# Performance work log

Hardware: AMD Instinct MI355X
Metric: run time of the kernel (lower is better)

The kernel has to match this reference:

```python
import jax, jax.numpy as jnp
import numpy as np

BETA = 0.25


def setup_inputs() -> dict:
    key = jax.random.key(0)
    k1, k2 = jax.random.split(key)
    z = jax.random.normal(k1, (32, 256, 32, 32), dtype=jnp.float32)
    codebook = jax.random.normal(k2, (1024, 256), dtype=jnp.float32)
    return {"z": z, "codebook": codebook}


def reference(z, codebook):
    # z: (B, C, H, W) with C == e_dim; codebook: (n_e, e_dim)
    b, c, h, w = z.shape
    z_perm = jnp.transpose(z, (0, 2, 3, 1))          # (B, H, W, C)
    z_flat = z_perm.reshape(-1, c)                   # (N, e_dim)

    d = (jnp.sum(z_flat ** 2, axis=1, keepdims=True)
         + jnp.sum(codebook ** 2, axis=1)
         - 2.0 * z_flat @ codebook.T)                # (N, n_e)

    min_idx = jnp.argmin(d, axis=1)                  # (N,)
    # gather == one-hot @ codebook in the original
    z_q = codebook[min_idx].reshape(z_perm.shape)    # (B, H, W, C)

    sg = jax.lax.stop_gradient
    e_latent_loss = jnp.mean((sg(z_q) - z_perm) ** 2)
    q_latent_loss = jnp.mean((z_q - sg(z_perm)) ** 2)
    codebook_loss = q_latent_loss + e_latent_loss * BETA

    # straight-through estimator
    z_q_st = z_perm + sg(z_q - z_perm)
    z_q_out = jnp.transpose(z_q_st, (0, 3, 1, 2))    # (B, C, H, W)

    indices = min_idx.reshape(b, 1, h, w)
    return z_q_out, codebook_loss, indices
```

## Files before the change

### kernel.cpp

```cpp
#include <hip/hip_runtime.h>


#define EDIM   256
#define NCODE  1024
#define HWSZ   1024
#define NPIX   32768
#define LOSS_OFF 8388608
#define IDX_OFF  8388609
#define THR    0.05f

typedef __attribute__((ext_vector_type(8))) short s16x8;
typedef __attribute__((ext_vector_type(4))) float f32x4;

__device__ inline unsigned short f2bf(float f) {
    unsigned u = __float_as_uint(f);
    return (unsigned short)((u + 0x7FFFu + ((u >> 16) & 1u)) >> 16);
}
__device__ inline float bf2f(unsigned short h) { return __uint_as_float(((unsigned)h) << 16); }

__global__ __launch_bounds__(256) void vq_cbsplit(const float* __restrict__ cb,
                                                  unsigned short* __restrict__ cbs,
                                                  float* __restrict__ cnorm)
{
    const int t    = threadIdx.x;
    const int code = (blockIdx.x << 3) + (t >> 5);
    const int kg   = t & 31;
    const float4 v0 = *(const float4*)(cb + (size_t)code * EDIM + (kg << 3));
    const float4 v1 = *(const float4*)(cb + (size_t)code * EDIM + (kg << 3) + 4);

    float s = v0.x*v0.x + v0.y*v0.y + v0.z*v0.z + v0.w*v0.w
            + v1.x*v1.x + v1.y*v1.y + v1.z*v1.z + v1.w*v1.w;
    s += __shfl_xor(s, 1, 64);  s += __shfl_xor(s, 2, 64);
    s += __shfl_xor(s, 4, 64);  s += __shfl_xor(s, 8, 64);
    s += __shfl_xor(s, 16, 64);
    if (kg == 0) cnorm[code] = s;

    const float f[8] = {v0.x, v0.y, v0.z, v0.w, v1.x, v1.y, v1.z, v1.w};
    unsigned short h[8], l[8];
#pragma unroll
    for (int j = 0; j < 8; ++j) { h[j] = f2bf(f[j]); l[j] = f2bf(f[j] - bf2f(h[j])); }
    uint4 H, L;
    H.x = (unsigned)h[0] | ((unsigned)h[1] << 16);  H.y = (unsigned)h[2] | ((unsigned)h[3] << 16);
    H.z = (unsigned)h[4] | ((unsigned)h[5] << 16);  H.w = (unsigned)h[6] | ((unsigned)h[7] << 16);
    L.x = (unsigned)l[0] | ((unsigned)l[1] << 16);  L.y = (unsigned)l[2] | ((unsigned)l[3] << 16);
    L.z = (unsigned)l[4] | ((unsigned)l[5] << 16);  L.w = (unsigned)l[6] | ((unsigned)l[7] << 16);
    const size_t off = ((size_t)(kg >> 2) * NCODE + code) * 64 + ((size_t)(kg & 3) << 3);
    *(uint4*)(cbs + off)      = H;
    *(uint4*)(cbs + off + 32) = L;
}

__global__ __launch_bounds__(256) void vq_prep(const float* __restrict__ z,
                                               unsigned short* __restrict__ zscH,
                                               unsigned short* __restrict__ zscL,
                                               float* __restrict__ loss_slot)
{
    __shared__ unsigned lzp[64][68];

    const int t  = threadIdx.x;
    const int n0 = blockIdx.x << 6;
    const int bb = n0 >> 10, hw0 = n0 & 1023;
    if (blockIdx.x == 0 && t == 0) *loss_slot = 0.0f;
    const float* zb = z + (size_t)bb * (EDIM * HWSZ) + hw0;

    for (int pk = 0; pk < 4; ++pk) {
#pragma unroll
        for (int i = 0; i < 4; ++i) {
            const int linear = (i << 8) + t;
            const int kk  = linear >> 4;
            const int px4 = (linear & 15) << 2;
            const float4 v = *reinterpret_cast<const float4*>(zb + (pk * 64 + kk) * HWSZ + px4);
            const float vv[4] = {v.x, v.y, v.z, v.w};
#pragma unroll
            for (int j = 0; j < 4; ++j) {
                const unsigned short h = f2bf(vv[j]);
                const unsigned short l = f2bf(vv[j] - bf2f(h));
                lzp[px4 + j][kk] = (unsigned)h | ((unsigned)l << 16);
            }
        }
        __syncthreads();
        {
            const int px = t >> 2, q = t & 3;
            const int kq16 = q << 4;
            const uint4 q0 = *(const uint4*)&lzp[px][kq16];
            const uint4 q1 = *(const uint4*)&lzp[px][kq16 + 4];
            const uint4 q2 = *(const uint4*)&lzp[px][kq16 + 8];
            const uint4 q3 = *(const uint4*)&lzp[px][kq16 + 12];
            #define PH(a,b) (((a) & 0xffffu) | ((b) << 16))
            #define PL(a,b) (((a) >> 16) | ((b) & 0xffff0000u))
            const uint4 hA = {PH(q0.x,q0.y), PH(q0.z,q0.w), PH(q1.x,q1.y), PH(q1.z,q1.w)};
            const uint4 hB = {PH(q2.x,q2.y), PH(q2.z,q2.w), PH(q3.x,q3.y), PH(q3.z,q3.w)};
            const uint4 lA = {PL(q0.x,q0.y), PL(q0.z,q0.w), PL(q1.x,q1.y), PL(q1.z,q1.w)};
            const uint4 lB = {PL(q2.x,q2.y), PL(q2.z,q2.w), PL(q3.x,q3.y), PL(q3.z,q3.w)};
            #undef PH
            #undef PL
            const int kc  = (pk << 1) + (q >> 1);
            const size_t off = ((size_t)kc * NPIX + n0 + px) * 32 + ((q & 1) << 4);
            *(uint4*)(zscH + off)     = hA;
            *(uint4*)(zscH + off + 8) = hB;
            *(uint4*)(zscL + off)     = lA;
            *(uint4*)(zscL + off + 8) = lB;
        }
        __syncthreads();
    }
}

__global__ __launch_bounds__(256, 2) void vq_argmin_g(
    const float* __restrict__ z, const float* __restrict__ cb,
    const unsigned short* __restrict__ zscH, const unsigned short* __restrict__ zscL,
    const unsigned short* __restrict__ cbs, const float* __restrict__ cnorm,
    float* __restrict__ idx_out)
{
    __shared__ unsigned short zh[8][64][32];
    __shared__ unsigned short zl[8][64][32];
    __shared__ float cn[NCODE];
    __shared__ float rb1[4][64], rb2[4][64];
    __shared__ int   ri1[4][64], ri2[4][64];
    __shared__ int   fl_cnt, fl_px[64], fl_i1[64], fl_i2[64];
    __shared__ float fred[2][4];

    const int t    = threadIdx.x;
    const int lane = t & 63;
    const int w    = t >> 6;
    const int n0   = blockIdx.x << 6;
    const int bb   = n0 >> 10, hw0 = n0 & 1023;
    const int l15  = lane & 15, kq = lane >> 4;

#pragma unroll
    for (int i = 0; i < 8; ++i) {
        const int idx = (i << 8) + t;
        const int kc  = idx >> 8;
        const int px  = (idx & 255) >> 2;
        const int q   = idx & 3;
        const size_t so = ((size_t)kc * NPIX + n0 + px) * 32 + (q << 3);
        *(uint4*)&zh[kc][px][q << 3] = *(const uint4*)(zscH + so);
        *(uint4*)&zl[kc][px][q << 3] = *(const uint4*)(zscL + so);
    }
#pragma unroll
    for (int i = 0; i < 4; ++i) cn[(i << 8) + t] = cnorm[(i << 8) + t];
    if (t == 0) fl_cnt = 0;
    __syncthreads();

    float b1[4], b2[4]; int i1[4], i2[4];
#pragma unroll
    for (int nf = 0; nf < 4; ++nf) { b1[nf] = 3.402823e38f; b2[nf] = 3.402823e38f; i1[nf] = 0; i2[nf] = 0; }

    f32x4 acc[4][4];
    const size_t lanebase = ((size_t)((w << 6) + l15) << 6) + (kq << 3);

    s16x8 pA0, pA1, pA2, pA3, pA4, pA5, pA6, pA7;
    s16x8 pB0, pB1, pB2, pB3, pB4, pB5, pB6, pB7;

#define LOADA(d0,d1,d2,d3,d4,d5,d6,d7,S) do {                                   \
        const int g_ = (S) >> 3, kc_ = (S) & 7;                                 \
        const unsigned short* bp = cbs +                                        \
            (((size_t)kc_ * NCODE + (g_ << 8)) << 6) + lanebase;                \
        d0 = *(const s16x8*)(bp);          d1 = *(const s16x8*)(bp + 1024);     \
        d2 = *(const s16x8*)(bp + 2048);   d3 = *(const s16x8*)(bp + 3072);     \
        d4 = *(const s16x8*)(bp + 32);     d5 = *(const s16x8*)(bp + 1056);     \
        d6 = *(const s16x8*)(bp + 2080);   d7 = *(const s16x8*)(bp + 3104);     \
    } while (0)

#define COMPUTE(a0,a1,a2,a3,a4,a5,a6,a7,S) do {                                 \
        const int g_ = (S) >> 3, kc_ = (S) & 7;                                 \
        if (kc_ == 0) {                                                         \
            _Pragma("unroll") for (int mf = 0; mf < 4; ++mf)                    \
            _Pragma("unroll") for (int nf = 0; nf < 4; ++nf)                    \
                acc[mf][nf] = (f32x4){0.f, 0.f, 0.f, 0.f};                      \
        }                                                                       \
        s16x8 bh[4], bl[4];                                                     \
        _Pragma("unroll") for (int nf = 0; nf < 4; ++nf) {                      \
            bh[nf] = *(const s16x8*)&zh[kc_][(nf << 4) + l15][kq << 3];         \
            bl[nf] = *(const s16x8*)&zl[kc_][(nf << 4) + l15][kq << 3];         \
        }                                                                       \
        _Pragma("unroll") for (int nf = 0; nf < 4; ++nf) {                      \
            acc[0][nf] = __builtin_amdgcn_mfma_f32_16x16x32_bf16(a0, bh[nf], acc[0][nf], 0, 0, 0); \
            acc[1][nf] = __builtin_amdgcn_mfma_f32_16x16x32_bf16(a1, bh[nf], acc[1][nf], 0, 0, 0); \
            acc[2][nf] = __builtin_amdgcn_mfma_f32_16x16x32_bf16(a2, bh[nf], acc[2][nf], 0, 0, 0); \
            acc[3][nf] = __builtin_amdgcn_mfma_f32_16x16x32_bf16(a3, bh[nf], acc[3][nf], 0, 0, 0); \
        }                                                                       \
        _Pragma("unroll") for (int nf = 0; nf < 4; ++nf) {                      \
            acc[0][nf] = __builtin_amdgcn_mfma_f32_16x16x32_bf16(a0, bl[nf], acc[0][nf], 0, 0, 0); \
            acc[1][nf] = __builtin_amdgcn_mfma_f32_16x16x32_bf16(a1, bl[nf], acc[1][nf], 0, 0, 0); \
            acc[2][nf] = __builtin_amdgcn_mfma_f32_16x16x32_bf16(a2, bl[nf], acc[2][nf], 0, 0, 0); \
            acc[3][nf] = __builtin_amdgcn_mfma_f32_16x16x32_bf16(a3, bl[nf], acc[3][nf], 0, 0, 0); \
        }                                                                       \
        _Pragma("unroll") for (int nf = 0; nf < 4; ++nf) {                      \
            acc[0][nf] = __builtin_amdgcn_mfma_f32_16x16x32_bf16(a4, bh[nf], acc[0][nf], 0, 0, 0); \
            acc[1][nf] = __builtin_amdgcn_mfma_f32_16x16x32_bf16(a5, bh[nf], acc[1][nf], 0, 0, 0); \
            acc[2][nf] = __builtin_amdgcn_mfma_f32_16x16x32_bf16(a6, bh[nf], acc[2][nf], 0, 0, 0); \
            acc[3][nf] = __builtin_amdgcn_mfma_f32_16x16x32_bf16(a7, bh[nf], acc[3][nf], 0, 0, 0); \
        }                                                                       \
        if (kc_ == 7) {                                                         \
            _Pragma("unroll") for (int mf = 0; mf < 4; ++mf)                    \
            _Pragma("unroll") for (int r = 0; r < 4; ++r) {                     \
                const int local = (w << 6) + (mf << 4) + (kq << 2) + r;         \
                const int code  = (g_ << 8) + local;                            \
                const float cnv = cn[code];                                     \
                _Pragma("unroll") for (int nf = 0; nf < 4; ++nf) {              \
                    const float d = fmaf(-2.f, acc[mf][nf][r], cnv);            \
                    if (d < b1[nf])      { b2[nf] = b1[nf]; i2[nf] = i1[nf]; b1[nf] = d; i1[nf] = code; } \
                    else if (d < b2[nf]) { b2[nf] = d; i2[nf] = code; }         \
                }                                                               \
            }                                                                   \
        }                                                                       \
    } while (0)

    LOADA(pA0,pA1,pA2,pA3,pA4,pA5,pA6,pA7, 0);
    for (int s = 0; s < 32; s += 2) {
        LOADA(pB0,pB1,pB2,pB3,pB4,pB5,pB6,pB7, s + 1);
        COMPUTE(pA0,pA1,pA2,pA3,pA4,pA5,pA6,pA7, s);
        if (s + 2 < 32) LOADA(pA0,pA1,pA2,pA3,pA4,pA5,pA6,pA7, s + 2);
        COMPUTE(pB0,pB1,pB2,pB3,pB4,pB5,pB6,pB7, s + 1);
    }
#undef LOADA
#undef COMPUTE

#pragma unroll
    for (int nf = 0; nf < 4; ++nf) {
        float B1 = b1[nf], B2 = b2[nf]; int I1 = i1[nf], I2 = i2[nf];
#pragma unroll
        for (int m = 16; m <= 32; m <<= 1) {
            const float ob1 = __shfl_xor(B1, m, 64), ob2 = __shfl_xor(B2, m, 64);
            const int   oi1 = __shfl_xor(I1, m, 64), oi2 = __shfl_xor(I2, m, 64);
            if (ob1 < B1 || (ob1 == B1 && oi1 < I1)) {
                if (B1 < ob2 || (B1 == ob2 && I1 < oi2)) { B2 = B1; I2 = I1; }
                else                                      { B2 = ob2; I2 = oi2; }
                B1 = ob1; I1 = oi1;
            } else if (ob1 < B2 || (ob1 == B2 && oi1 < I2)) { B2 = ob1; I2 = oi1; }
        }
        if (lane < 16) {
            const int px = (nf << 4) + lane;
            rb1[w][px] = B1; rb2[w][px] = B2; ri1[w][px] = I1; ri2[w][px] = I2;
        }
    }
    __syncthreads();
    if (t < 64) {
        float B1 = rb1[0][t], B2 = rb2[0][t]; int I1 = ri1[0][t], I2 = ri2[0][t];
#pragma unroll
        for (int ww = 1; ww < 4; ++ww) {
            const float ob1 = rb1[ww][t], ob2 = rb2[ww][t];
            const int   oi1 = ri1[ww][t], oi2 = ri2[ww][t];
            if (ob1 < B1 || (ob1 == B1 && oi1 < I1)) {
                if (B1 < ob2 || (B1 == ob2 && I1 < oi2)) { B2 = B1; I2 = I1; }
                else                                      { B2 = ob2; I2 = oi2; }
                B1 = ob1; I1 = oi1;
            } else if (ob1 < B2 || (ob1 == B2 && oi1 < I2)) { B2 = ob1; I2 = oi1; }
        }
        if (B2 - B1 > THR) idx_out[n0 + t] = (float)I1;
        else {
            const int pos = atomicAdd(&fl_cnt, 1);
            fl_px[pos] = t; fl_i1[pos] = I1; fl_i2[pos] = I2;
        }
    }
    __syncthreads();
    const int nfl = fl_cnt;
    for (int fi = 0; fi < nfl; ++fi) {
        const int px = fl_px[fi], ia = fl_i1[fi], ib = fl_i2[fi];
        const float zk = z[(size_t)bb * (EDIM * HWSZ) + t * HWSZ + hw0 + px];
        const float da = zk - cb[(size_t)ia * EDIM + t];
        const float db = zk - cb[(size_t)ib * EDIM + t];
        float s1 = da * da, s2 = db * db;
#pragma unroll
        for (int m = 32; m; m >>= 1) { s1 += __shfl_xor(s1, m, 64); s2 += __shfl_xor(s2, m, 64); }
        if (lane == 0) { fred[0][w] = s1; fred[1][w] = s2; }
        __syncthreads();
        if (t == 0) {
            const float d1 = fred[0][0] + fred[0][1] + fred[0][2] + fred[0][3];
            const float d2 = fred[1][0] + fred[1][1] + fred[1][2] + fred[1][3];
            const int win = (d2 < d1 || (d2 == d1 && ib < ia)) ? ib : ia;
            idx_out[n0 + px] = (float)win;
        }
        __syncthreads();
    }
}

__global__ __launch_bounds__(256) void vq_gather(const float* __restrict__ z,
                                                 const float* __restrict__ cb,
                                                 const float* __restrict__ idxf,
                                                 float* __restrict__ out)
{
    __shared__ float lq[64][129];
    __shared__ int   sidx[64];

    const int t   = threadIdx.x;
    const int n0  = blockIdx.x << 6;
    const int bb  = n0 >> 10;
    const int hw0 = n0 & 1023;

    if (t < 64) sidx[t] = (int)idxf[n0 + t];

    const float* zb = z   + (size_t)bb * (EDIM * HWSZ) + hw0;
    float*       ob = out + (size_t)bb * (EDIM * HWSZ) + hw0;
    const int p  = t & 63;
    const int cq = t >> 6;
    float sum = 0.0f;

    for (int h = 0; h < 2; ++h) {
        __syncthreads();
#pragma unroll
        for (int i = 0; i < 8; ++i) {
            const int linear = (i << 8) + t;
            const int pr = linear >> 5;
            const int f4 = (linear & 31) << 2;
            const float4 v = *reinterpret_cast<const float4*>(
                cb + (size_t)sidx[pr] * EDIM + (h << 7) + f4);
            float* dst = &lq[pr][f4];
            dst[0] = v.x; dst[1] = v.y; dst[2] = v.z; dst[3] = v.w;
        }
        __syncthreads();
#pragma unroll 4
        for (int r = 0; r < 32; ++r) {
            const int c  = (r << 2) + cq;
            const int cf = (h << 7) + c;
            const float q  = lq[p][c];
            const float zv = zb[cf * HWSZ + p];
            ob[cf * HWSZ + p] = q;
            const float dd = q - zv;
            sum = fmaf(dd, dd, sum);
        }
    }

#pragma unroll
    for (int m = 32; m; m >>= 1) sum += __shfl_xor(sum, m, 64);
    if (p == 0) atomicAdd(out + LOSS_OFF, sum * (1.25f / 8388608.0f));
}

extern "C" void kernel_launch(void* const* d_in, const int* in_sizes, int n_in,
                              void* d_out, int out_size, void* d_ws, size_t ws_size,
                              hipStream_t stream)
{
    const float* z  = (const float*)d_in[0];
    const float* cb = (const float*)d_in[1];
    float* out = (float*)d_out;
    unsigned short* zscH = (unsigned short*)out;
    unsigned short* zscL = zscH + (size_t)8 * NPIX * 32;
    unsigned short* cbs = (unsigned short*)d_ws;
    float*          cnp = (float*)(cbs + (size_t)8 * NCODE * 64);

    vq_cbsplit <<<NCODE / 8, 256, 0, stream>>>(cb, cbs, cnp);
    vq_prep    <<<NPIX / 64, 256, 0, stream>>>(z, zscH, zscL, out + LOSS_OFF);
    vq_argmin_g<<<NPIX / 64, 256, 0, stream>>>(z, cb, zscH, zscL, cbs, cnp, out + IDX_OFF);
    vq_gather  <<<NPIX / 64, 256, 0, stream>>>(z, cb, out + IDX_OFF, out);
}
```

Baseline: 203.4 us.

## Fuse z split, argmin and gather into one kernel; split codebook planes

Merges the z bf16 hi/lo split, the MFMA argmin and the gather/loss pass into one kernel per 64-pixel tile. The split z is written straight into shared memory instead of going through a global scratch buffer, and the chosen indices stay in shared memory for the gather. This removes two launches and the global round trip of the split z. The codebook hi/lo halves now live in separate planes, and the loss reset moves into the codebook kernel. The catch is that the fused kernel reads z twice and reuses the zh shared buffer as gather staging, which could cost some occupancy or overlap.

```diff
diff --git a/kernel.cpp b/kernel.cpp
--- a/kernel.cpp
+++ b/kernel.cpp
@@ -19,12 +19,15 @@
 __device__ inline float bf2f(unsigned short h) { return __uint_as_float(((unsigned)h) << 16); }
 
 __global__ __launch_bounds__(256) void vq_cbsplit(const float* __restrict__ cb,
-                                                  unsigned short* __restrict__ cbs,
-                                                  float* __restrict__ cnorm)
+                                                  unsigned short* __restrict__ cbsH,
+                                                  unsigned short* __restrict__ cbsL,
+                                                  float* __restrict__ cnorm,
+                                                  float* __restrict__ loss_slot)
 {
     const int t    = threadIdx.x;
     const int code = (blockIdx.x << 3) + (t >> 5);
     const int kg   = t & 31;
+    if (blockIdx.x == 0 && t == 0) *loss_slot = 0.0f;
     const float4 v0 = *(const float4*)(cb + (size_t)code * EDIM + (kg << 3));
     const float4 v1 = *(const float4*)(cb + (size_t)code * EDIM + (kg << 3) + 4);
 
@@ -44,71 +47,15 @@
     H.z = (unsigned)h[4] | ((unsigned)h[5] << 16);  H.w = (unsigned)h[6] | ((unsigned)h[7] << 16);
     L.x = (unsigned)l[0] | ((unsigned)l[1] << 16);  L.y = (unsigned)l[2] | ((unsigned)l[3] << 16);
     L.z = (unsigned)l[4] | ((unsigned)l[5] << 16);  L.w = (unsigned)l[6] | ((unsigned)l[7] << 16);
-    const size_t off = ((size_t)(kg >> 2) * NCODE + code) * 64 + ((size_t)(kg & 3) << 3);
-    *(uint4*)(cbs + off)      = H;
-    *(uint4*)(cbs + off + 32) = L;
-}
-
-__global__ __launch_bounds__(256) void vq_prep(const float* __restrict__ z,
-                                               unsigned short* __restrict__ zscH,
-                                               unsigned short* __restrict__ zscL,
-                                               float* __restrict__ loss_slot)
-{
-    __shared__ unsigned lzp[64][68];
-
-    const int t  = threadIdx.x;
-    const int n0 = blockIdx.x << 6;
-    const int bb = n0 >> 10, hw0 = n0 & 1023;
-    if (blockIdx.x == 0 && t == 0) *loss_slot = 0.0f;
-    const float* zb = z + (size_t)bb * (EDIM * HWSZ) + hw0;
-
-    for (int pk = 0; pk < 4; ++pk) {
-#pragma unroll
-        for (int i = 0; i < 4; ++i) {
-            const int linear = (i << 8) + t;
-            const int kk  = linear >> 4;
-            const int px4 = (linear & 15) << 2;
-            const float4 v = *reinterpret_cast<const float4*>(zb + (pk * 64 + kk) * HWSZ + px4);
-            const float vv[4] = {v.x, v.y, v.z, v.w};
-#pragma unroll
-            for (int j = 0; j < 4; ++j) {
-                const unsigned short h = f2bf(vv[j]);
-                const unsigned short l = f2bf(vv[j] - bf2f(h));
-                lzp[px4 + j][kk] = (unsigned)h | ((unsigned)l << 16);
-            }
-        }
-        __syncthreads();
-        {
-            const int px = t >> 2, q = t & 3;
-            const int kq16 = q << 4;
-            const uint4 q0 = *(const uint4*)&lzp[px][kq16];
-            const uint4 q1 = *(const uint4*)&lzp[px][kq16 + 4];
-            const uint4 q2 = *(const uint4*)&lzp[px][kq16 + 8];
-            const uint4 q3 = *(const uint4*)&lzp[px][kq16 + 12];
-            #define PH(a,b) (((a) & 0xffffu) | ((b) << 16))
-            #define PL(a,b) (((a) >> 16) | ((b) & 0xffff0000u))
-            const uint4 hA = {PH(q0.x,q0.y), PH(q0.z,q0.w), PH(q1.x,q1.y), PH(q1.z,q1.w)};
-            const uint4 hB = {PH(q2.x,q2.y), PH(q2.z,q2.w), PH(q3.x,q3.y), PH(q3.z,q3.w)};
-            const uint4 lA = {PL(q0.x,q0.y), PL(q0.z,q0.w), PL(q1.x,q1.y), PL(q1.z,q1.w)};
-            const uint4 lB = {PL(q2.x,q2.y), PL(q2.z,q2.w), PL(q3.x,q3.y), PL(q3.z,q3.w)};
-            #undef PH
-            #undef PL
-            const int kc  = (pk << 1) + (q >> 1);
-            const size_t off = ((size_t)kc * NPIX + n0 + px) * 32 + ((q & 1) << 4);
-            *(uint4*)(zscH + off)     = hA;
-            *(uint4*)(zscH + off + 8) = hB;
-            *(uint4*)(zscL + off)     = lA;
-            *(uint4*)(zscL + off + 8) = lB;
-        }
-        __syncthreads();
-    }
-}
-
-__global__ __launch_bounds__(256, 2) void vq_argmin_g(
+    const size_t off = ((size_t)(kg >> 2) * NCODE + code) * 32 + ((size_t)(kg & 3) << 3);
+    *(uint4*)(cbsH + off) = H;
+    *(uint4*)(cbsL + off) = L;
+}
+
+__global__ __launch_bounds__(256, 2) void vq_mega(
     const float* __restrict__ z, const float* __restrict__ cb,
-    const unsigned short* __restrict__ zscH, const unsigned short* __restrict__ zscL,
-    const unsigned short* __restrict__ cbs, const float* __restrict__ cnorm,
-    float* __restrict__ idx_out)
+    const unsigned short* __restrict__ cbsH, const unsigned short* __restrict__ cbsL,
+    const float* __restrict__ cnorm, float* __restrict__ out)
 {
     __shared__ unsigned short zh[8][64][32];
     __shared__ unsigned short zl[8][64][32];
@@ -117,6 +64,7 @@
     __shared__ int   ri1[4][64], ri2[4][64];
     __shared__ int   fl_cnt, fl_px[64], fl_i1[64], fl_i2[64];
     __shared__ float fred[2][4];
+    __shared__ int   sidx[64];
 
     const int t    = threadIdx.x;
     const int lane = t & 63;
@@ -125,15 +73,24 @@
     const int bb   = n0 >> 10, hw0 = n0 & 1023;
     const int l15  = lane & 15, kq = lane >> 4;
 
-#pragma unroll
-    for (int i = 0; i < 8; ++i) {
-        const int idx = (i << 8) + t;
-        const int kc  = idx >> 8;
-        const int px  = (idx & 255) >> 2;
-        const int q   = idx & 3;
-        const size_t so = ((size_t)kc * NPIX + n0 + px) * 32 + (q << 3);
-        *(uint4*)&zh[kc][px][q << 3] = *(const uint4*)(zscH + so);
-        *(uint4*)&zl[kc][px][q << 3] = *(const uint4*)(zscL + so);
+    const float* zb = z   + (size_t)bb * (EDIM * HWSZ) + hw0;
+    float*       ob = out + (size_t)bb * (EDIM * HWSZ) + hw0;
+
+#pragma unroll 4
+    for (int i = 0; i < 16; ++i) {
+        const int linear = (i << 8) + t;
+        const int c   = linear >> 4;
+        const int px4 = (linear & 15) << 2;
+        const float4 v = *(const float4*)(zb + c * HWSZ + px4);
+        const float vv[4] = {v.x, v.y, v.z, v.w};
+        const int kc = c >> 5, ko = c & 31;
+#pragma unroll
+        for (int j = 0; j < 4; ++j) {
+            const unsigned short h = f2bf(vv[j]);
+            const unsigned short l = f2bf(vv[j] - bf2f(h));
+            zh[kc][px4 + j][ko] = h;
+            zl[kc][px4 + j][ko] = l;
+        }
     }
 #pragma unroll
     for (int i = 0; i < 4; ++i) cn[(i << 8) + t] = cnorm[(i << 8) + t];
@@ -145,19 +102,20 @@
     for (int nf = 0; nf < 4; ++nf) { b1[nf] = 3.402823e38f; b2[nf] = 3.402823e38f; i1[nf] = 0; i2[nf] = 0; }
 
     f32x4 acc[4][4];
-    const size_t lanebase = ((size_t)((w << 6) + l15) << 6) + (kq << 3);
+    const size_t lanebase = ((size_t)((w << 6) + l15) << 5) + (kq << 3);
 
     s16x8 pA0, pA1, pA2, pA3, pA4, pA5, pA6, pA7;
     s16x8 pB0, pB1, pB2, pB3, pB4, pB5, pB6, pB7;
 
 #define LOADA(d0,d1,d2,d3,d4,d5,d6,d7,S) do {                                   \
         const int g_ = (S) >> 3, kc_ = (S) & 7;                                 \
-        const unsigned short* bp = cbs +                                        \
-            (((size_t)kc_ * NCODE + (g_ << 8)) << 6) + lanebase;                \
-        d0 = *(const s16x8*)(bp);          d1 = *(const s16x8*)(bp + 1024);     \
-        d2 = *(const s16x8*)(bp + 2048);   d3 = *(const s16x8*)(bp + 3072);     \
-        d4 = *(const s16x8*)(bp + 32);     d5 = *(const s16x8*)(bp + 1056);     \
-        d6 = *(const s16x8*)(bp + 2080);   d7 = *(const s16x8*)(bp + 3104);     \
+        const size_t tb = (((size_t)kc_ * NCODE + (g_ << 8)) << 5) + lanebase;  \
+        const unsigned short* bpH = cbsH + tb;                                  \
+        const unsigned short* bpL = cbsL + tb;                                  \
+        d0 = *(const s16x8*)(bpH);         d1 = *(const s16x8*)(bpH + 512);     \
+        d2 = *(const s16x8*)(bpH + 1024);  d3 = *(const s16x8*)(bpH + 1536);    \
+        d4 = *(const s16x8*)(bpL);         d5 = *(const s16x8*)(bpL + 512);     \
+        d6 = *(const s16x8*)(bpL + 1024);  d7 = *(const s16x8*)(bpL + 1536);    \
     } while (0)
 
 #define COMPUTE(a0,a1,a2,a3,a4,a5,a6,a7,S) do {                                 \
@@ -246,8 +204,10 @@
                 B1 = ob1; I1 = oi1;
             } else if (ob1 < B2 || (ob1 == B2 && oi1 < I2)) { B2 = ob1; I2 = oi1; }
         }
-        if (B2 - B1 > THR) idx_out[n0 + t] = (float)I1;
-        else {
+        if (B2 - B1 > THR) {
+            out[IDX_OFF + n0 + t] = (float)I1;
+            sidx[t] = I1;
+        } else {
             const int pos = atomicAdd(&fl_cnt, 1);
             fl_px[pos] = t; fl_i1[pos] = I1; fl_i2[pos] = I2;
         }
@@ -268,61 +228,44 @@
             const float d1 = fred[0][0] + fred[0][1] + fred[0][2] + fred[0][3];
             const float d2 = fred[1][0] + fred[1][1] + fred[1][2] + fred[1][3];
             const int win = (d2 < d1 || (d2 == d1 && ib < ia)) ? ib : ia;
-            idx_out[n0 + px] = (float)win;
-        }
-        __syncthreads();
-    }
-}
-
-__global__ __launch_bounds__(256) void vq_gather(const float* __restrict__ z,
-                                                 const float* __restrict__ cb,
-                                                 const float* __restrict__ idxf,
-                                                 float* __restrict__ out)
-{
-    __shared__ float lq[64][129];
-    __shared__ int   sidx[64];
-
-    const int t   = threadIdx.x;
-    const int n0  = blockIdx.x << 6;
-    const int bb  = n0 >> 10;
-    const int hw0 = n0 & 1023;
-
-    if (t < 64) sidx[t] = (int)idxf[n0 + t];
-
-    const float* zb = z   + (size_t)bb * (EDIM * HWSZ) + hw0;
-    float*       ob = out + (size_t)bb * (EDIM * HWSZ) + hw0;
+            out[IDX_OFF + n0 + px] = (float)win;
+            sidx[px] = win;
+        }
+        __syncthreads();
+    }
+
+    float* lqf = (float*)&zh[0][0][0];
     const int p  = t & 63;
     const int cq = t >> 6;
     float sum = 0.0f;
 
-    for (int h = 0; h < 2; ++h) {
-        __syncthreads();
-#pragma unroll
-        for (int i = 0; i < 8; ++i) {
+    for (int h4 = 0; h4 < 4; ++h4) {
+        __syncthreads();
+#pragma unroll
+        for (int i = 0; i < 4; ++i) {
             const int linear = (i << 8) + t;
-            const int pr = linear >> 5;
-            const int f4 = (linear & 31) << 2;
-            const float4 v = *reinterpret_cast<const float4*>(
-                cb + (size_t)sidx[pr] * EDIM + (h << 7) + f4);
-            float* dst = &lq[pr][f4];
+            const int pr = linear >> 4;
+            const int f4 = (linear & 15) << 2;
+            const float4 v = *(const float4*)(
+                cb + (size_t)sidx[pr] * EDIM + (h4 << 6) + f4);
+            float* dst = &lqf[pr * 65 + f4];
             dst[0] = v.x; dst[1] = v.y; dst[2] = v.z; dst[3] = v.w;
         }
         __syncthreads();
 #pragma unroll 4
-        for (int r = 0; r < 32; ++r) {
+        for (int r = 0; r < 16; ++r) {
             const int c  = (r << 2) + cq;
-            const int cf = (h << 7) + c;
-            const float q  = lq[p][c];
+            const int cf = (h4 << 6) + c;
+            const float q  = lqf[p * 65 + c];
             const float zv = zb[cf * HWSZ + p];
             ob[cf * HWSZ + p] = q;
             const float dd = q - zv;
             sum = fmaf(dd, dd, sum);
         }
     }
-
 #pragma unroll
     for (int m = 32; m; m >>= 1) sum += __shfl_xor(sum, m, 64);
-    if (p == 0) atomicAdd(out + LOSS_OFF, sum * (1.25f / 8388608.0f));
+    if (lane == 0) atomicAdd(out + LOSS_OFF, sum * (1.25f / 8388608.0f));
 }
 
 extern "C" void kernel_launch(void* const* d_in, const int* in_sizes, int n_in,
@@ -332,13 +275,11 @@
     const float* z  = (const float*)d_in[0];
     const float* cb = (const float*)d_in[1];
     float* out = (float*)d_out;
-    unsigned short* zscH = (unsigned short*)out;
-    unsigned short* zscL = zscH + (size_t)8 * NPIX * 32;
-    unsigned short* cbs = (unsigned short*)d_ws;
-    float*          cnp = (float*)(cbs + (size_t)8 * NCODE * 64);
-
-    vq_cbsplit <<<NCODE / 8, 256, 0, stream>>>(cb, cbs, cnp);
-    vq_prep    <<<NPIX / 64, 256, 0, stream>>>(z, zscH, zscL, out + LOSS_OFF);
-    vq_argmin_g<<<NPIX / 64, 256, 0, stream>>>(z, cb, zscH, zscL, cbs, cnp, out + IDX_OFF);
-    vq_gather  <<<NPIX / 64, 256, 0, stream>>>(z, cb, out + IDX_OFF, out);
-}
+    const size_t plane = (size_t)8 * NCODE * 32;
+    unsigned short* cbsH = (unsigned short*)d_ws;
+    unsigned short* cbsL = cbsH + plane;
+    float*          cnp  = (float*)(cbsL + plane);
+
+    vq_cbsplit<<<NCODE / 8, 256, 0, stream>>>(cb, cbsH, cbsL, cnp, out + LOSS_OFF);
+    vq_mega   <<<NPIX / 64, 256, 0, stream>>>(z, cb, cbsH, cbsL, cnp, out);
+}
```

Result: faster. 168.4 us (-17.2%).
